# Kernel tuning notes

Measured on AMD Instinct MI355X. Metric: run time of the kernel, lower is better.

Reference implementation:

```python
import jax, jax.numpy as jnp
import numpy as np
from jax import lax

B = 32768
IMG = 28
K = 3
OUT_HW = IMG - K + 1  # 26
FLAT = OUT_HW * OUT_HW  # 676
HID = 300
NCLS = 10


def setup_inputs() -> dict:
    key = jax.random.key(0)
    ks = jax.random.split(key, 8)
    x = jax.random.normal(ks[0], (B, IMG * IMG), dtype=jnp.float32)
    conv_w = jax.random.normal(ks[1], (K, K), dtype=jnp.float32) * 0.1
    # Linear params stored as (in, out) so forward is h @ W + b
    W1 = jax.random.normal(ks[2], (FLAT, HID), dtype=jnp.float32) * 0.04
    b1 = jnp.zeros((HID,), dtype=jnp.float32)
    W2 = jax.random.normal(ks[3], (HID, HID), dtype=jnp.float32) * 0.06
    b2 = jnp.zeros((HID,), dtype=jnp.float32)
    W3 = jax.random.normal(ks[4], (HID, NCLS), dtype=jnp.float32) * 0.06
    b3 = jnp.zeros((NCLS,), dtype=jnp.float32)
    return {"x": x, "conv_w": conv_w, "W1": W1, "b1": b1,
            "W2": W2, "b2": b2, "W3": W3, "b3": b3}


def reference(x, conv_w, W1, b1, W2, b2, W3, b3):
    b = x.shape[0]
    img = x.reshape(b, 1, IMG, IMG)  # NCHW
    # Valid cross-correlation with 3x3 kernel -> [B,1,26,26]
    y = lax.conv_general_dilated(
        img, conv_w[None, None, :, :], window_strides=(1, 1), padding="VALID",
        dimension_numbers=("NCHW", "OIHW", "NCHW"))
    h = y.reshape(b, FLAT)
    h = jax.nn.relu(h @ W1 + b1)
    h = jax.nn.relu(h @ W2 + b2)
    return h @ W3 + b3
```

## Files before the change

### kernel.cpp

```cpp
#include <hip/hip_runtime.h>


typedef __bf16 bf16_t;
typedef __bf16 bf16x8 __attribute__((ext_vector_type(8)));
typedef float  f32x4  __attribute__((ext_vector_type(4)));

#define MFMA16(a, b, c) __builtin_amdgcn_mfma_f32_16x16x32_bf16((a), (b), (c), 0, 0, 0)

#define W1F_ELEMS (25 * 20 * 64 * 8)
#define W2F_ELEMS (10 * 20 * 64 * 8)
#define W3F_ELEMS (10 * 1 * 64 * 8)
#define H1_OFF    768000
#define H1_BYTES  ((size_t)32768 * 320 * 2)

__global__ void prep_weights(const float* __restrict__ conv_w,
                             const float* __restrict__ W1,
                             const float* __restrict__ W2,
                             const float* __restrict__ W3,
                             bf16_t* __restrict__ W1f,
                             bf16_t* __restrict__ W2f,
                             bf16_t* __restrict__ W3f) {
    int idx = blockIdx.x * 256 + threadIdx.x;
    if (idx < 800 * 320) {
        int k = idx / 320;
        int n = idx - k * 320;
        float v = 0.0f;
        if (k < 784 && n < 300) {
            int py = k / 28;
            int px = k - py * 28;
#pragma unroll
            for (int ky = 0; ky < 3; ++ky) {
                int oy = py - ky;
                if (oy < 0 || oy > 25) continue;
#pragma unroll
                for (int kx = 0; kx < 3; ++kx) {
                    int ox = px - kx;
                    if (ox < 0 || ox > 25) continue;
                    v += conv_w[ky * 3 + kx] * W1[(oy * 26 + ox) * 300 + n];
                }
            }
        }
        int kc = k >> 5, quad = (k >> 3) & 3, j = k & 7;
        int nt = n >> 4, nin = n & 15;
        W1f[(((kc * 20 + nt) * 64 + quad * 16 + nin) << 3) + j] = (bf16_t)v;
    } else if (idx < 800 * 320 + 320 * 320) {
        int i2 = idx - 800 * 320;
        int k = i2 / 320;
        int n = i2 - k * 320;
        float v = (k < 300 && n < 300) ? W2[k * 300 + n] : 0.0f;
        int kc = k >> 5, quad = (k >> 3) & 3, j = k & 7;
        int nt = n >> 4, nin = n & 15;
        W2f[(((kc * 20 + nt) * 64 + quad * 16 + nin) << 3) + j] = (bf16_t)v;
    } else if (idx < 800 * 320 + 320 * 320 + 320 * 16) {
        int i3 = idx - (800 * 320 + 320 * 320);
        int k = i3 / 16;
        int n = i3 - k * 16;
        float v = (k < 300 && n < 10) ? W3[k * 10 + n] : 0.0f;
        int kc = k >> 5, quad = (k >> 3) & 3, j = k & 7;
        W3f[(((kc * 64) + quad * 16 + n) << 3) + j] = (bf16_t)v;
    }
}

__device__ __forceinline__ void stage16(const bf16x8* g, bf16x8* l) {
    __builtin_amdgcn_global_load_lds(
        (const __attribute__((address_space(1))) void*)g,
        (__attribute__((address_space(3))) void*)l, 16, 0, 0);
}

__global__ __launch_bounds__(512, 4) void gemm1(
    const float* __restrict__ x, const float* __restrict__ b1,
    const bf16x8* __restrict__ W1f, bf16_t* __restrict__ h1) {
    __shared__ bf16x8 bufB[2 * 1280];

    const int tid = threadIdx.x;
    const int w   = tid >> 6;
    const int l   = tid & 63;
    const int mh  = w & 1;
    const int nq  = w >> 1;
    const int q   = l >> 4;
    const int l15 = l & 15;
    const int r0  = blockIdx.x * 64;

    const float* rowA = x + (size_t)(r0 + mh * 32 + l15) * 784;
    const float* rowB = rowA + 16 * 784;

    for (int t = w; t < 20; t += 8) stage16(W1f + (t * 64 + l), bufB + t * 64);
    float4 ua0, ua1, ub0, ub1;
    {
        const float4* pa = (const float4*)(rowA + q * 8);
        const float4* pb = (const float4*)(rowB + q * 8);
        ua0 = pa[0]; ua1 = pa[1]; ub0 = pb[0]; ub1 = pb[1];
    }

    f32x4 acc[2][5];
#pragma unroll
    for (int m = 0; m < 2; ++m)
#pragma unroll
        for (int nt = 0; nt < 5; ++nt) acc[m][nt] = (f32x4){0.f, 0.f, 0.f, 0.f};

    for (int kc = 0; kc < 25; ++kc) {
        __syncthreads();

        if (kc + 1 < 25) {
            int s1 = (kc + 1) & 1;
            for (int t = w; t < 20; t += 8)
                stage16(W1f + (((kc + 1) * 20 + t) * 64 + l),
                        bufB + s1 * 1280 + t * 64);
        }

        bf16x8 afA, afB;
        afA[0] = (bf16_t)ua0.x; afA[1] = (bf16_t)ua0.y;
        afA[2] = (bf16_t)ua0.z; afA[3] = (bf16_t)ua0.w;
        afA[4] = (bf16_t)ua1.x; afA[5] = (bf16_t)ua1.y;
        afA[6] = (bf16_t)ua1.z; afA[7] = (bf16_t)ua1.w;
        afB[0] = (bf16_t)ub0.x; afB[1] = (bf16_t)ub0.y;
        afB[2] = (bf16_t)ub0.z; afB[3] = (bf16_t)ub0.w;
        afB[4] = (bf16_t)ub1.x; afB[5] = (bf16_t)ub1.y;
        afB[6] = (bf16_t)ub1.z; afB[7] = (bf16_t)ub1.w;

        if (kc + 1 < 25) {
            int k0 = (kc + 1) * 32 + q * 8;
            if (k0 < 784) {
                const float4* pa = (const float4*)(rowA + k0);
                const float4* pb = (const float4*)(rowB + k0);
                ua0 = pa[0]; ua1 = pa[1]; ub0 = pb[0]; ub1 = pb[1];
            } else {
                ua0 = ua1 = ub0 = ub1 = make_float4(0.f, 0.f, 0.f, 0.f);
            }
        }

        const bf16x8* bb = bufB + (kc & 1) * 1280 + (nq * 5) * 64 + l;
#pragma unroll
        for (int nt = 0; nt < 5; ++nt) {
            bf16x8 b = bb[nt * 64];
            acc[0][nt] = MFMA16(afA, b, acc[0][nt]);
            acc[1][nt] = MFMA16(afB, b, acc[1][nt]);
        }
    }

#pragma unroll
    for (int nt = 0; nt < 5; ++nt) {
        int n = (nq * 5 + nt) * 16 + l15;
        float bias = (n < 300) ? b1[n] : 0.0f;
#pragma unroll
        for (int mt2 = 0; mt2 < 2; ++mt2) {
            int mt = mh * 2 + mt2;
#pragma unroll
            for (int r = 0; r < 4; ++r) {
                float v = acc[mt2][nt][r] + bias;
                v = v > 0.f ? v : 0.f;
                h1[(size_t)(r0 + mt * 16 + q * 4 + r) * 320 + n] = (bf16_t)v;
            }
        }
    }
}

__global__ __launch_bounds__(512, 4) void gemm23(
    const bf16_t* __restrict__ h1, const float* __restrict__ b2,
    const float* __restrict__ b3, const bf16x8* __restrict__ W2f,
    const bf16x8* __restrict__ W3f, float* __restrict__ out) {
    __shared__ bf16x8 arena[2560];

    const int tid = threadIdx.x;
    const int w   = tid >> 6;
    const int l   = tid & 63;
    const int mh  = w & 1;
    const int nq  = w >> 1;
    const int q   = l >> 4;
    const int l15 = l & 15;
    const int r0  = blockIdx.x * 64;

    const bf16_t* rowA = h1 + (size_t)(r0 + mh * 32 + l15) * 320;
    const bf16_t* rowB = rowA + 16 * 320;

    for (int t = w; t < 20; t += 8) stage16(W2f + (t * 64 + l), arena + t * 64);
    bf16x8 uaA = *(const bf16x8*)(rowA + q * 8);
    bf16x8 uaB = *(const bf16x8*)(rowB + q * 8);

    f32x4 acc[2][5];
#pragma unroll
    for (int m = 0; m < 2; ++m)
#pragma unroll
        for (int nt = 0; nt < 5; ++nt) acc[m][nt] = (f32x4){0.f, 0.f, 0.f, 0.f};

    for (int kc = 0; kc < 10; ++kc) {
        __syncthreads();

        if (kc + 1 < 10) {
            int s1 = (kc + 1) & 1;
            for (int t = w; t < 20; t += 8)
                stage16(W2f + (((kc + 1) * 20 + t) * 64 + l),
                        arena + s1 * 1280 + t * 64);
        }

        bf16x8 afA = uaA, afB = uaB;
        if (kc + 1 < 10) {
            uaA = *(const bf16x8*)(rowA + (kc + 1) * 32 + q * 8);
            uaB = *(const bf16x8*)(rowB + (kc + 1) * 32 + q * 8);
        }

        const bf16x8* bb = arena + (kc & 1) * 1280 + (nq * 5) * 64 + l;
#pragma unroll
        for (int nt = 0; nt < 5; ++nt) {
            bf16x8 b = bb[nt * 64];
            acc[0][nt] = MFMA16(afA, b, acc[0][nt]);
            acc[1][nt] = MFMA16(afB, b, acc[1][nt]);
        }
    }
    __syncthreads();

    {
        bf16_t* hb = (bf16_t*)arena;
#pragma unroll
        for (int nt = 0; nt < 5; ++nt) {
            int n = (nq * 5 + nt) * 16 + l15;
            float bias = (n < 300) ? b2[n] : 0.0f;
            int kc2 = n >> 5, quad = (n >> 3) & 3, j = n & 7;
#pragma unroll
            for (int mt2 = 0; mt2 < 2; ++mt2) {
                int mt = mh * 2 + mt2;
#pragma unroll
                for (int r = 0; r < 4; ++r) {
                    float v = acc[mt2][nt][r] + bias;
                    v = v > 0.f ? v : 0.f;
                    hb[(((kc2 * 4 + mt) * 64 + quad * 16 + q * 4 + r) << 3) + j] =
                        (bf16_t)v;
                }
            }
        }
    }
    __syncthreads();

    if (w < 4) {
        f32x4 acc3 = (f32x4){0.f, 0.f, 0.f, 0.f};
        for (int kc = 0; kc < 10; ++kc) {
            bf16x8 a = arena[(kc * 4 + w) * 64 + l];
            bf16x8 b = W3f[kc * 64 + l];
            acc3 = MFMA16(a, b, acc3);
        }
        if (l15 < 10) {
            float bias = b3[l15];
#pragma unroll
            for (int r = 0; r < 4; ++r)
                out[(size_t)(r0 + w * 16 + q * 4 + r) * 10 + l15] = acc3[r] + bias;
        }
    }
}

extern "C" void kernel_launch(void* const* d_in, const int* in_sizes, int n_in,
                              void* d_out, int out_size, void* d_ws, size_t ws_size,
                              hipStream_t stream) {
    const float* x      = (const float*)d_in[0];
    const float* conv_w = (const float*)d_in[1];
    const float* W1     = (const float*)d_in[2];
    const float* b1     = (const float*)d_in[3];
    const float* W2     = (const float*)d_in[4];
    const float* b2     = (const float*)d_in[5];
    const float* W3     = (const float*)d_in[6];
    const float* b3     = (const float*)d_in[7];
    float* out = (float*)d_out;

    char* ws = (char*)d_ws;
    bf16_t* W1f = (bf16_t*)(ws);
    bf16_t* W2f = (bf16_t*)(ws + (size_t)W1F_ELEMS * 2);
    bf16_t* W3f = (bf16_t*)(ws + (size_t)(W1F_ELEMS + W2F_ELEMS) * 2);
    bf16_t* h1  = (bf16_t*)(ws + H1_OFF);
    if (ws_size < H1_OFF + H1_BYTES) return;

    int prep_total = 800 * 320 + 320 * 320 + 320 * 16;
    prep_weights<<<(prep_total + 255) / 256, 256, 0, stream>>>(
        conv_w, W1, W2, W3, W1f, W2f, W3f);

    gemm1<<<32768 / 64, 512, 0, stream>>>(x, b1, (const bf16x8*)W1f, h1);

    gemm23<<<32768 / 64, 512, 0, stream>>>(
        h1, b2, b3, (const bf16x8*)W2f, (const bf16x8*)W3f, out);
}
```

Baseline: 215.8 us.

## Load weight fragments directly into registers instead of LDS staging

Both GEMM kernels drop the global_load_lds staging of weight tiles and the per-iteration barriers. Each wave instead loads its 10 B fragments straight from global (L2) into double-buffered registers, with fully unrolled k-loops. Blocks shrink from 512 to 256 threads, and each wave now covers 10 N-tiles instead of 5. This removes LDS traffic and sync overhead, at the cost of much higher register pressure (40 accumulators plus double-buffered operands), lower occupancy, and redundant weight loads across waves sharing the same N group.

```diff
diff --git a/kernel.cpp b/kernel.cpp
--- a/kernel.cpp
+++ b/kernel.cpp
@@ -61,164 +61,153 @@
     }
 }
 
-__device__ __forceinline__ void stage16(const bf16x8* g, bf16x8* l) {
-    __builtin_amdgcn_global_load_lds(
-        (const __attribute__((address_space(1))) void*)g,
-        (__attribute__((address_space(3))) void*)l, 16, 0, 0);
-}
-
-__global__ __launch_bounds__(512, 4) void gemm1(
+__global__ __launch_bounds__(256, 2) void gemm1(
     const float* __restrict__ x, const float* __restrict__ b1,
     const bf16x8* __restrict__ W1f, bf16_t* __restrict__ h1) {
-    __shared__ bf16x8 bufB[2 * 1280];
-
     const int tid = threadIdx.x;
     const int w   = tid >> 6;
     const int l   = tid & 63;
-    const int mh  = w & 1;
-    const int nq  = w >> 1;
+    const int mg  = w & 1;
+    const int ng  = w >> 1;
     const int q   = l >> 4;
     const int l15 = l & 15;
     const int r0  = blockIdx.x * 64;
 
-    const float* rowA = x + (size_t)(r0 + mh * 32 + l15) * 784;
+    const float* rowA = x + (size_t)(r0 + mg * 32 + l15) * 784;
     const float* rowB = rowA + 16 * 784;
-
-    for (int t = w; t < 20; t += 8) stage16(W1f + (t * 64 + l), bufB + t * 64);
-    float4 ua0, ua1, ub0, ub1;
+    const bf16x8* wbase = W1f + ng * 10 * 64 + l;
+
+    float4 abuf[2][4];
+    bf16x8 bbuf[2][10];
+    f32x4  acc[2][10];
+#pragma unroll
+    for (int m = 0; m < 2; ++m)
+#pragma unroll
+        for (int nt = 0; nt < 10; ++nt) acc[m][nt] = (f32x4){0.f, 0.f, 0.f, 0.f};
+
     {
         const float4* pa = (const float4*)(rowA + q * 8);
         const float4* pb = (const float4*)(rowB + q * 8);
-        ua0 = pa[0]; ua1 = pa[1]; ub0 = pb[0]; ub1 = pb[1];
-    }
-
-    f32x4 acc[2][5];
-#pragma unroll
-    for (int m = 0; m < 2; ++m)
-#pragma unroll
-        for (int nt = 0; nt < 5; ++nt) acc[m][nt] = (f32x4){0.f, 0.f, 0.f, 0.f};
-
+        abuf[0][0] = pa[0]; abuf[0][1] = pa[1];
+        abuf[0][2] = pb[0]; abuf[0][3] = pb[1];
+#pragma unroll
+        for (int nt = 0; nt < 10; ++nt) bbuf[0][nt] = wbase[nt * 64];
+    }
+
+#pragma unroll
     for (int kc = 0; kc < 25; ++kc) {
-        __syncthreads();
-
-        if (kc + 1 < 25) {
-            int s1 = (kc + 1) & 1;
-            for (int t = w; t < 20; t += 8)
-                stage16(W1f + (((kc + 1) * 20 + t) * 64 + l),
-                        bufB + s1 * 1280 + t * 64);
-        }
-
-        bf16x8 afA, afB;
-        afA[0] = (bf16_t)ua0.x; afA[1] = (bf16_t)ua0.y;
-        afA[2] = (bf16_t)ua0.z; afA[3] = (bf16_t)ua0.w;
-        afA[4] = (bf16_t)ua1.x; afA[5] = (bf16_t)ua1.y;
-        afA[6] = (bf16_t)ua1.z; afA[7] = (bf16_t)ua1.w;
-        afB[0] = (bf16_t)ub0.x; afB[1] = (bf16_t)ub0.y;
-        afB[2] = (bf16_t)ub0.z; afB[3] = (bf16_t)ub0.w;
-        afB[4] = (bf16_t)ub1.x; afB[5] = (bf16_t)ub1.y;
-        afB[6] = (bf16_t)ub1.z; afB[7] = (bf16_t)ub1.w;
-
-        if (kc + 1 < 25) {
+        const int cur = kc & 1, nxt = cur ^ 1;
+
+        if (kc < 24) {
             int k0 = (kc + 1) * 32 + q * 8;
             if (k0 < 784) {
                 const float4* pa = (const float4*)(rowA + k0);
                 const float4* pb = (const float4*)(rowB + k0);
-                ua0 = pa[0]; ua1 = pa[1]; ub0 = pb[0]; ub1 = pb[1];
+                abuf[nxt][0] = pa[0]; abuf[nxt][1] = pa[1];
+                abuf[nxt][2] = pb[0]; abuf[nxt][3] = pb[1];
             } else {
-                ua0 = ua1 = ub0 = ub1 = make_float4(0.f, 0.f, 0.f, 0.f);
-            }
-        }
-
-        const bf16x8* bb = bufB + (kc & 1) * 1280 + (nq * 5) * 64 + l;
-#pragma unroll
-        for (int nt = 0; nt < 5; ++nt) {
-            bf16x8 b = bb[nt * 64];
-            acc[0][nt] = MFMA16(afA, b, acc[0][nt]);
-            acc[1][nt] = MFMA16(afB, b, acc[1][nt]);
-        }
-    }
-
-#pragma unroll
-    for (int nt = 0; nt < 5; ++nt) {
-        int n = (nq * 5 + nt) * 16 + l15;
+                abuf[nxt][0] = abuf[nxt][1] = abuf[nxt][2] = abuf[nxt][3] =
+                    make_float4(0.f, 0.f, 0.f, 0.f);
+            }
+            const bf16x8* wb = wbase + (kc + 1) * 20 * 64;
+#pragma unroll
+            for (int nt = 0; nt < 10; ++nt) bbuf[nxt][nt] = wb[nt * 64];
+        }
+
+        bf16x8 afA, afB;
+        afA[0] = (bf16_t)abuf[cur][0].x; afA[1] = (bf16_t)abuf[cur][0].y;
+        afA[2] = (bf16_t)abuf[cur][0].z; afA[3] = (bf16_t)abuf[cur][0].w;
+        afA[4] = (bf16_t)abuf[cur][1].x; afA[5] = (bf16_t)abuf[cur][1].y;
+        afA[6] = (bf16_t)abuf[cur][1].z; afA[7] = (bf16_t)abuf[cur][1].w;
+        afB[0] = (bf16_t)abuf[cur][2].x; afB[1] = (bf16_t)abuf[cur][2].y;
+        afB[2] = (bf16_t)abuf[cur][2].z; afB[3] = (bf16_t)abuf[cur][2].w;
+        afB[4] = (bf16_t)abuf[cur][3].x; afB[5] = (bf16_t)abuf[cur][3].y;
+        afB[6] = (bf16_t)abuf[cur][3].z; afB[7] = (bf16_t)abuf[cur][3].w;
+
+#pragma unroll
+        for (int nt = 0; nt < 10; ++nt) {
+            acc[0][nt] = MFMA16(afA, bbuf[cur][nt], acc[0][nt]);
+            acc[1][nt] = MFMA16(afB, bbuf[cur][nt], acc[1][nt]);
+        }
+    }
+
+#pragma unroll
+    for (int nt = 0; nt < 10; ++nt) {
+        int n = (ng * 10 + nt) * 16 + l15;
         float bias = (n < 300) ? b1[n] : 0.0f;
 #pragma unroll
         for (int mt2 = 0; mt2 < 2; ++mt2) {
-            int mt = mh * 2 + mt2;
+            int row_base = r0 + (mg * 2 + mt2) * 16 + q * 4;
 #pragma unroll
             for (int r = 0; r < 4; ++r) {
                 float v = acc[mt2][nt][r] + bias;
                 v = v > 0.f ? v : 0.f;
-                h1[(size_t)(r0 + mt * 16 + q * 4 + r) * 320 + n] = (bf16_t)v;
-            }
-        }
-    }
-}
-
-__global__ __launch_bounds__(512, 4) void gemm23(
+                h1[(size_t)(row_base + r) * 320 + n] = (bf16_t)v;
+            }
+        }
+    }
+}
+
+__global__ __launch_bounds__(256, 2) void gemm23(
     const bf16_t* __restrict__ h1, const float* __restrict__ b2,
     const float* __restrict__ b3, const bf16x8* __restrict__ W2f,
     const bf16x8* __restrict__ W3f, float* __restrict__ out) {
-    __shared__ bf16x8 arena[2560];
+    __shared__ bf16x8 hx[10 * 4 * 64];
 
     const int tid = threadIdx.x;
     const int w   = tid >> 6;
     const int l   = tid & 63;
-    const int mh  = w & 1;
-    const int nq  = w >> 1;
+    const int mg  = w & 1;
+    const int ng  = w >> 1;
     const int q   = l >> 4;
     const int l15 = l & 15;
     const int r0  = blockIdx.x * 64;
 
-    const bf16_t* rowA = h1 + (size_t)(r0 + mh * 32 + l15) * 320;
+    const bf16_t* rowA = h1 + (size_t)(r0 + mg * 32 + l15) * 320;
     const bf16_t* rowB = rowA + 16 * 320;
-
-    for (int t = w; t < 20; t += 8) stage16(W2f + (t * 64 + l), arena + t * 64);
-    bf16x8 uaA = *(const bf16x8*)(rowA + q * 8);
-    bf16x8 uaB = *(const bf16x8*)(rowB + q * 8);
-
-    f32x4 acc[2][5];
+    const bf16x8* wbase = W2f + ng * 10 * 64 + l;
+
+    bf16x8 adbuf[2][2];
+    bf16x8 bbuf[2][10];
+    f32x4  acc[2][10];
 #pragma unroll
     for (int m = 0; m < 2; ++m)
 #pragma unroll
-        for (int nt = 0; nt < 5; ++nt) acc[m][nt] = (f32x4){0.f, 0.f, 0.f, 0.f};
-
+        for (int nt = 0; nt < 10; ++nt) acc[m][nt] = (f32x4){0.f, 0.f, 0.f, 0.f};
+
+    adbuf[0][0] = *(const bf16x8*)(rowA + q * 8);
+    adbuf[0][1] = *(const bf16x8*)(rowB + q * 8);
+#pragma unroll
+    for (int nt = 0; nt < 10; ++nt) bbuf[0][nt] = wbase[nt * 64];
+
+#pragma unroll
     for (int kc = 0; kc < 10; ++kc) {
-        __syncthreads();
-
-        if (kc + 1 < 10) {
-            int s1 = (kc + 1) & 1;
-            for (int t = w; t < 20; t += 8)
-                stage16(W2f + (((kc + 1) * 20 + t) * 64 + l),
-                        arena + s1 * 1280 + t * 64);
-        }
-
-        bf16x8 afA = uaA, afB = uaB;
-        if (kc + 1 < 10) {
-            uaA = *(const bf16x8*)(rowA + (kc + 1) * 32 + q * 8);
-            uaB = *(const bf16x8*)(rowB + (kc + 1) * 32 + q * 8);
-        }
-
-        const bf16x8* bb = arena + (kc & 1) * 1280 + (nq * 5) * 64 + l;
-#pragma unroll
-        for (int nt = 0; nt < 5; ++nt) {
-            bf16x8 b = bb[nt * 64];
-            acc[0][nt] = MFMA16(afA, b, acc[0][nt]);
-            acc[1][nt] = MFMA16(afB, b, acc[1][nt]);
-        }
-    }
-    __syncthreads();
+        const int cur = kc & 1, nxt = cur ^ 1;
+        if (kc < 9) {
+            int k0 = (kc + 1) * 32 + q * 8;
+            adbuf[nxt][0] = *(const bf16x8*)(rowA + k0);
+            adbuf[nxt][1] = *(const bf16x8*)(rowB + k0);
+            const bf16x8* wb = wbase + (kc + 1) * 20 * 64;
+#pragma unroll
+            for (int nt = 0; nt < 10; ++nt) bbuf[nxt][nt] = wb[nt * 64];
+        }
+#pragma unroll
+        for (int nt = 0; nt < 10; ++nt) {
+            acc[0][nt] = MFMA16(adbuf[cur][0], bbuf[cur][nt], acc[0][nt]);
+            acc[1][nt] = MFMA16(adbuf[cur][1], bbuf[cur][nt], acc[1][nt]);
+        }
+    }
 
     {
-        bf16_t* hb = (bf16_t*)arena;
-#pragma unroll
-        for (int nt = 0; nt < 5; ++nt) {
-            int n = (nq * 5 + nt) * 16 + l15;
+        bf16_t* hb = (bf16_t*)hx;
+#pragma unroll
+        for (int nt = 0; nt < 10; ++nt) {
+            int n = (ng * 10 + nt) * 16 + l15;
             float bias = (n < 300) ? b2[n] : 0.0f;
             int kc2 = n >> 5, quad = (n >> 3) & 3, j = n & 7;
 #pragma unroll
             for (int mt2 = 0; mt2 < 2; ++mt2) {
-                int mt = mh * 2 + mt2;
+                int mt = mg * 2 + mt2;
 #pragma unroll
                 for (int r = 0; r < 4; ++r) {
                     float v = acc[mt2][nt][r] + bias;
@@ -231,19 +220,15 @@
     }
     __syncthreads();
 
-    if (w < 4) {
-        f32x4 acc3 = (f32x4){0.f, 0.f, 0.f, 0.f};
-        for (int kc = 0; kc < 10; ++kc) {
-            bf16x8 a = arena[(kc * 4 + w) * 64 + l];
-            bf16x8 b = W3f[kc * 64 + l];
-            acc3 = MFMA16(a, b, acc3);
-        }
-        if (l15 < 10) {
-            float bias = b3[l15];
-#pragma unroll
-            for (int r = 0; r < 4; ++r)
-                out[(size_t)(r0 + w * 16 + q * 4 + r) * 10 + l15] = acc3[r] + bias;
-        }
+    f32x4 acc3 = (f32x4){0.f, 0.f, 0.f, 0.f};
+#pragma unroll
+    for (int kc = 0; kc < 10; ++kc)
+        acc3 = MFMA16(hx[(kc * 4 + w) * 64 + l], W3f[kc * 64 + l], acc3);
+    if (l15 < 10) {
+        float bias = b3[l15];
+#pragma unroll
+        for (int r = 0; r < 4; ++r)
+            out[(size_t)(r0 + w * 16 + q * 4 + r) * 10 + l15] = acc3[r] + bias;
     }
 }
 
@@ -271,8 +256,8 @@
     prep_weights<<<(prep_total + 255) / 256, 256, 0, stream>>>(
         conv_w, W1, W2, W3, W1f, W2f, W3f);
 
-    gemm1<<<32768 / 64, 512, 0, stream>>>(x, b1, (const bf16x8*)W1f, h1);
-
-    gemm23<<<32768 / 64, 512, 0, stream>>>(
+    gemm1<<<32768 / 64, 256, 0, stream>>>(x, b1, (const bf16x8*)W1f, h1);
+
+    gemm23<<<32768 / 64, 256, 0, stream>>>(
         h1, b2, b3, (const bf16x8*)W2f, (const bf16x8*)W3f, out);
 }
```

New measurement: 232.6 us. +7.8%, slower.

## Stage x tiles through LDS with coalesced loads in gemm1

Applied to the files above, without the earlier changes.

Replaces each wave's per-lane strided float4 reads of x (duplicated across the four N-quarter waves) with a block-cooperative coalesced load of 128-column bands. Each band is converted to bf16 once and written to a padded LDS tile, and the MFMA A fragments are then read from LDS. This removes redundant global reads of x and improves coalescing. In exchange it adds an LDS buffer (lower occupancy headroom) and an extra barrier per band.

```diff
diff --git a/kernel.cpp b/kernel.cpp
--- a/kernel.cpp
+++ b/kernel.cpp
@@ -2,6 +2,7 @@
 
 
 typedef __bf16 bf16_t;
+typedef __bf16 bf16x4 __attribute__((ext_vector_type(4)));
 typedef __bf16 bf16x8 __attribute__((ext_vector_type(8)));
 typedef float  f32x4  __attribute__((ext_vector_type(4)));
 
@@ -12,6 +13,7 @@
 #define W3F_ELEMS (10 * 1 * 64 * 8)
 #define H1_OFF    768000
 #define H1_BYTES  ((size_t)32768 * 320 * 2)
+#define ASTRIDE   136
 
 __global__ void prep_weights(const float* __restrict__ conv_w,
                              const float* __restrict__ W1,
@@ -71,6 +73,7 @@
     const float* __restrict__ x, const float* __restrict__ b1,
     const bf16x8* __restrict__ W1f, bf16_t* __restrict__ h1) {
     __shared__ bf16x8 bufB[2 * 1280];
+    __shared__ bf16_t Abuf[64 * ASTRIDE];
 
     const int tid = threadIdx.x;
     const int w   = tid >> 6;
@@ -81,16 +84,17 @@
     const int l15 = l & 15;
     const int r0  = blockIdx.x * 64;
 
-    const float* rowA = x + (size_t)(r0 + mh * 32 + l15) * 784;
-    const float* rowB = rowA + 16 * 784;
+    const int srow = tid >> 5;
+    const int sc4  = tid & 31;
+    const int trow = tid >> 3;
+    const int tc4  = tid & 7;
 
     for (int t = w; t < 20; t += 8) stage16(W1f + (t * 64 + l), bufB + t * 64);
-    float4 ua0, ua1, ub0, ub1;
-    {
-        const float4* pa = (const float4*)(rowA + q * 8);
-        const float4* pb = (const float4*)(rowB + q * 8);
-        ua0 = pa[0]; ua1 = pa[1]; ub0 = pb[0]; ub1 = pb[1];
-    }
+
+    float4 pf[4];
+#pragma unroll
+    for (int i = 0; i < 4; ++i)
+        pf[i] = *(const float4*)(x + (size_t)(r0 + i * 16 + srow) * 784 + sc4 * 4);
 
     f32x4 acc[2][5];
 #pragma unroll
@@ -98,43 +102,58 @@
 #pragma unroll
         for (int nt = 0; nt < 5; ++nt) acc[m][nt] = (f32x4){0.f, 0.f, 0.f, 0.f};
 
-    for (int kc = 0; kc < 25; ++kc) {
+    int kc = 0;
+    for (int band = 0; band < 7; ++band) {
         __syncthreads();
 
-        if (kc + 1 < 25) {
-            int s1 = (kc + 1) & 1;
-            for (int t = w; t < 20; t += 8)
-                stage16(W1f + (((kc + 1) * 20 + t) * 64 + l),
-                        bufB + s1 * 1280 + t * 64);
-        }
-
-        bf16x8 afA, afB;
-        afA[0] = (bf16_t)ua0.x; afA[1] = (bf16_t)ua0.y;
-        afA[2] = (bf16_t)ua0.z; afA[3] = (bf16_t)ua0.w;
-        afA[4] = (bf16_t)ua1.x; afA[5] = (bf16_t)ua1.y;
-        afA[6] = (bf16_t)ua1.z; afA[7] = (bf16_t)ua1.w;
-        afB[0] = (bf16_t)ub0.x; afB[1] = (bf16_t)ub0.y;
-        afB[2] = (bf16_t)ub0.z; afB[3] = (bf16_t)ub0.w;
-        afB[4] = (bf16_t)ub1.x; afB[5] = (bf16_t)ub1.y;
-        afB[6] = (bf16_t)ub1.z; afB[7] = (bf16_t)ub1.w;
-
-        if (kc + 1 < 25) {
-            int k0 = (kc + 1) * 32 + q * 8;
-            if (k0 < 784) {
-                const float4* pa = (const float4*)(rowA + k0);
-                const float4* pb = (const float4*)(rowB + k0);
-                ua0 = pa[0]; ua1 = pa[1]; ub0 = pb[0]; ub1 = pb[1];
-            } else {
-                ua0 = ua1 = ub0 = ub1 = make_float4(0.f, 0.f, 0.f, 0.f);
-            }
-        }
-
-        const bf16x8* bb = bufB + (kc & 1) * 1280 + (nq * 5) * 64 + l;
-#pragma unroll
-        for (int nt = 0; nt < 5; ++nt) {
-            bf16x8 b = bb[nt * 64];
-            acc[0][nt] = MFMA16(afA, b, acc[0][nt]);
-            acc[1][nt] = MFMA16(afB, b, acc[1][nt]);
+        if (band < 6) {
+#pragma unroll
+            for (int i = 0; i < 4; ++i) {
+                bf16x4 v;
+                v[0] = (bf16_t)pf[i].x; v[1] = (bf16_t)pf[i].y;
+                v[2] = (bf16_t)pf[i].z; v[3] = (bf16_t)pf[i].w;
+                *(bf16x4*)&Abuf[(i * 16 + srow) * ASTRIDE + sc4 * 4] = v;
+            }
+        } else {
+            bf16x4 v;
+            v[0] = (bf16_t)pf[0].x; v[1] = (bf16_t)pf[0].y;
+            v[2] = (bf16_t)pf[0].z; v[3] = (bf16_t)pf[0].w;
+            *(bf16x4*)&Abuf[trow * ASTRIDE + tc4 * 4] = v;
+        }
+
+        if (band + 1 < 6) {
+#pragma unroll
+            for (int i = 0; i < 4; ++i)
+                pf[i] = *(const float4*)(x + (size_t)(r0 + i * 16 + srow) * 784 +
+                                         (band + 1) * 128 + sc4 * 4);
+        } else if (band + 1 == 6) {
+            pf[0] = (tc4 < 4)
+                ? *(const float4*)(x + (size_t)(r0 + trow) * 784 + 768 + tc4 * 4)
+                : make_float4(0.f, 0.f, 0.f, 0.f);
+        }
+
+        const int nch = (band < 6) ? 4 : 1;
+        for (int kcl = 0; kcl < nch; ++kcl, ++kc) {
+            __syncthreads();
+
+            if (kc + 1 < 25) {
+                int s1 = (kc + 1) & 1;
+                for (int t = w; t < 20; t += 8)
+                    stage16(W1f + (((kc + 1) * 20 + t) * 64 + l),
+                            bufB + s1 * 1280 + t * 64);
+            }
+
+            bf16x8 afA = *(const bf16x8*)&Abuf[(mh * 32 + l15) * ASTRIDE +
+                                               kcl * 32 + q * 8];
+            bf16x8 afB = *(const bf16x8*)&Abuf[(mh * 32 + 16 + l15) * ASTRIDE +
+                                               kcl * 32 + q * 8];
+            const bf16x8* bb = bufB + (kc & 1) * 1280 + (nq * 5) * 64 + l;
+#pragma unroll
+            for (int nt = 0; nt < 5; ++nt) {
+                bf16x8 b = bb[nt * 64];
+                acc[0][nt] = MFMA16(afA, b, acc[0][nt]);
+                acc[1][nt] = MFMA16(afB, b, acc[1][nt]);
+            }
         }
     }
 
```

Measured after the change: 198.1 us. 1.09x faster.
